# Optimization experiments

Measured on AMD Instinct MI355X. Metric: run time of the kernel, lower is better.

The kernel has to match this reference:

```python
import jax, jax.numpy as jnp
import numpy as np

VOCAB = 50000
EDIM = 128
CDIM = 128
B = 512
LEVEL_FACTORS = [4, 4, 3, 3, 2, 1]  # 7 levels total, N = 403968 nodes


def _build_forest():
    """Deterministic random forest: per-level arrays of token, global parent idx, depth, batch id."""
    rng = np.random.default_rng(0)
    level_sizes = [B]
    for f in LEVEL_FACTORS:
        level_sizes.append(level_sizes[-1] * f)
    offsets = np.cumsum([0] + level_sizes)
    tokens = [rng.integers(0, VOCAB, B)]
    parent = [np.zeros(B, np.int64)]          # roots: dummy parent (depth 0 never scattered)
    depth = [np.zeros(B, np.int64)]
    batch_id = [np.arange(B)]
    for d in range(1, len(level_sizes)):
        n = level_sizes[d]
        tokens.append(rng.integers(0, VOCAB, n))
        p_local = rng.integers(0, level_sizes[d - 1], n)
        parent.append(offsets[d - 1] + p_local)
        depth.append(np.full(n, d, np.int64))
        batch_id.append(batch_id[d - 1][p_local])
    cat = lambda xs: np.concatenate(xs).astype(np.int32)
    return cat(tokens), cat(parent), cat(depth), cat(batch_id), len(level_sizes)


def setup_inputs() -> dict:
    key = jax.random.key(0)
    k1, k2, k3 = jax.random.split(key, 3)
    emb_table = jax.random.normal(k1, (VOCAB, EDIM), dtype=jnp.float32) * 0.02
    W = jax.random.normal(k2, (CDIM, EDIM), dtype=jnp.float32) * 0.02
    b = jax.random.normal(k3, (CDIM,), dtype=jnp.float32) * 0.02
    tokens, parent, depth, batch_id, num_levels = _build_forest()
    return {
        "emb_table": emb_table,
        "W": W,
        "b": b,
        "tokens": jnp.asarray(tokens),
        "parent": jnp.asarray(parent),
        "depth": jnp.asarray(depth),
        "batch_id": jnp.asarray(batch_id),
        "num_levels": num_levels,
        "batch_size": B,
    }


def reference(emb_table, W, b, tokens, parent, depth, batch_id, num_levels, batch_size):
    N = tokens.shape[0]
    # per-node base: W_c(embedding(token))  [N, CDIM]
    base = emb_table[tokens] @ W.T + b
    h = base
    # bottom-up subtree sum, level-batched scatter-add (deepest level first)
    for d in range(num_levels - 1, 0, -1):
        contrib = jnp.where((depth == d)[:, None], h, 0.0)
        h = h + jax.ops.segment_sum(contrib, parent, num_segments=N)
    # per-batch elementwise max over all nodes of the tree, clamped at 0
    # (original maxes zero-initialized snapshots over all recursion calls)
    out = jax.ops.segment_max(h, batch_id, num_segments=batch_size)
    return jnp.maximum(out, 0.0)
```

## Files before the change

kernel.cpp:

```cpp
#include <hip/hip_runtime.h>
#include <hip/hip_bf16.h>


using f32x4   = __attribute__((ext_vector_type(4))) float;
using short8  = __attribute__((ext_vector_type(8))) short;
using ushort8 = __attribute__((ext_vector_type(8))) unsigned short;
using float4v = __attribute__((ext_vector_type(4))) float;

#define N_ALL   403968
#define N_NONRT 403456
#define N_PAR   256512
#define OFF1    512
#define OFF2    2560
#define OFF3    10752
#define OFF4    35328
#define OFF5    109056
#define OFF6    256512
#define NVOCAB  50000
#define CAP1    32
#define CAP2    32
#define CAP3    24
#define CAP4    24
#define CAP5    20
#define CAPL    16
#define D1CAP   24
#define D2CAP   64
#define WEMB_BLOCKS 782

__device__ __forceinline__ short f2bf(float f) {
  union { float f; unsigned u; } v; v.f = f;
  unsigned r = v.u + 0x7fffu + ((v.u >> 16) & 1u);
  return (short)(r >> 16);
}
__device__ __forceinline__ float bf2f(unsigned short u) {
  union { unsigned u; float f; } v; v.u = ((unsigned)u) << 16; return v.f;
}

__global__ __launch_bounds__(256) void prep_k(const float* __restrict__ W,
                                              const float* __restrict__ emb,
                                              const float* __restrict__ bias,
                                              unsigned short* __restrict__ Wemb,
                                              const int* __restrict__ parent,
                                              const int* __restrict__ tokens,
                                              int* __restrict__ cnt,
                                              int* __restrict__ L1,
                                              int* __restrict__ L2,
                                              int* __restrict__ L3,
                                              int* __restrict__ L4,
                                              unsigned long long* __restrict__ L5,
                                              unsigned short* __restrict__ LeafTok) {
  if (blockIdx.x >= WEMB_BLOCKS) {
    const int i = (blockIdx.x - WEMB_BLOCKS) * 256 + threadIdx.x + 512;
    const int p = parent[i];
    const int slot = atomicAdd(cnt + p, 1);
    if (i >= OFF6) {
      if (slot < CAPL)
        LeafTok[(size_t)(p - OFF5) * CAPL + slot] = (unsigned short)tokens[i];
    } else if (i >= OFF5) {
      if (slot < CAP5) {
        const unsigned long long v =
            ((unsigned long long)(unsigned)tokens[i] << 32) |
            (unsigned)(i - OFF5);
        L5[(size_t)(p - OFF4) * CAP5 + slot] = v;
      }
    } else if (i >= OFF4) {
      if (slot < CAP4) L4[(size_t)(p - OFF3) * CAP4 + slot] = i - OFF4;
    } else if (i >= OFF3) {
      if (slot < CAP3) L3[(size_t)(p - OFF2) * CAP3 + slot] = i - OFF3;
    } else if (i >= OFF2) {
      if (slot < CAP2) L2[(size_t)(p - OFF1) * CAP2 + slot] = i - OFF2;
    } else {
      if (slot < CAP1) L1[(size_t)p * CAP1 + slot] = i - OFF1;
    }
    return;
  }
  __shared__ short WBs[16384];
  for (int idx = threadIdx.x; idx < 16384; idx += 256) {
    int j = idx & 7, c16 = (idx >> 3) & 15, g = (idx >> 7) & 3,
        s = (idx >> 9) & 3, t = idx >> 11;
    WBs[idx] = f2bf(W[(t * 16 + c16) * 128 + s * 32 + g * 8 + j]);
  }
  __syncthreads();

  const int tid = threadIdx.x, lane = tid & 63, wv = tid >> 6;
  const int l15 = lane & 15, g = lane >> 4;
  const int nb = blockIdx.x * 64 + wv * 16;

  f32x4 acc[8];
  #pragma unroll
  for (int t = 0; t < 8; ++t) {
    const float bb = bias[t * 16 + l15];
    #pragma unroll
    for (int j = 0; j < 4; ++j) acc[t][j] = bb;
  }
  int vr = nb + l15; if (vr > NVOCAB - 1) vr = NVOCAB - 1;
  const float* erow = emb + (size_t)vr * 128;
  short8 a[4];
  #pragma unroll
  for (int s = 0; s < 4; ++s) {
    float4v f0 = *(const float4v*)(erow + s * 32 + g * 8);
    float4v f1 = *(const float4v*)(erow + s * 32 + g * 8 + 4);
    short8 t;
    t[0] = f2bf(f0[0]); t[1] = f2bf(f0[1]); t[2] = f2bf(f0[2]); t[3] = f2bf(f0[3]);
    t[4] = f2bf(f1[0]); t[5] = f2bf(f1[1]); t[6] = f2bf(f1[2]); t[7] = f2bf(f1[3]);
    a[s] = t;
  }
  #pragma unroll
  for (int t = 0; t < 8; ++t) {
    #pragma unroll
    for (int s = 0; s < 4; ++s) {
      const short8 bfr = *(const short8*)&WBs[((((t * 4 + s) * 4) + g) * 16 + l15) * 8];
      acc[t] = __builtin_amdgcn_mfma_f32_16x16x32_bf16(a[s], bfr, acc[t], 0, 0, 0);
    }
  }
  #pragma unroll
  for (int j = 0; j < 4; ++j) {
    const int r = nb + g * 4 + j;
    if (r < NVOCAB) {
      ushort8 hv;
      #pragma unroll
      for (int t = 0; t < 8; ++t) hv[t] = (unsigned short)f2bf(acc[t][j]);
      *(ushort8*)(Wemb + (size_t)r * 128 + l15 * 8) = hv;
    }
  }
}

__global__ __launch_bounds__(256, 8) void d4f_k(
    const unsigned short* __restrict__ Wemb,
    const int*   __restrict__ tokens,
    const int*   __restrict__ cnt,
    const unsigned long long* __restrict__ L5,
    const unsigned short* __restrict__ LeafTok,
    unsigned short* __restrict__ Hout)
{
  const int chunk = threadIdx.x & 15;
  const int node  = threadIdx.x >> 4;
  const int nd    = blockIdx.x * 16 + node;
  const int gid   = OFF4 + nd;

  float acc[8], mx[8];
  {
    const int tok = tokens[gid];
    const ushort8 b = *(const ushort8*)(Wemb + (size_t)tok * 128 + chunk * 8);
    #pragma unroll
    for (int t = 0; t < 8; ++t) { acc[t] = bf2f(b[t]); mx[t] = 0.0f; }
  }

  const int n5 = min(cnt[gid], CAP5);
  const size_t b5 = (size_t)nd * CAP5;
  for (int c = 0; c < n5; ++c) {
    const unsigned long long e5 = L5[b5 + c];
    const int tok5 = (int)(e5 >> 32);
    const int lid5 = (int)(e5 & 0xffffffffu);
    const int lc = min(cnt[OFF5 + lid5], CAPL);
    const size_t lb = (size_t)lid5 * CAPL;
    const ushort8 r5 = *(const ushort8*)(Wemb + (size_t)tok5 * 128 + chunk * 8);
    float h5[8], lmx[8];
    #pragma unroll
    for (int t = 0; t < 8; ++t) { h5[t] = bf2f(r5[t]); lmx[t] = 0.0f; }
    for (int l = 0; l < lc; ++l) {
      const int tl = LeafTok[lb + l];
      const ushort8 rl = *(const ushort8*)(Wemb + (size_t)tl * 128 + chunk * 8);
      #pragma unroll
      for (int t = 0; t < 8; ++t) {
        const float hv = bf2f(rl[t]);
        h5[t] += hv;
        lmx[t] = fmaxf(lmx[t], hv);
      }
    }
    #pragma unroll
    for (int t = 0; t < 8; ++t) {
      acc[t] += h5[t];
      mx[t] = fmaxf(mx[t], fmaxf(lmx[t], h5[t]));
    }
  }

  ushort8 hv, mv;
  #pragma unroll
  for (int t = 0; t < 8; ++t) {
    hv[t] = (unsigned short)f2bf(acc[t]);
    mv[t] = (unsigned short)f2bf(fmaxf(mx[t], acc[t]));
  }
  __builtin_nontemporal_store(hv, (ushort8*)(Hout + (size_t)nd * 256 + chunk * 8));
  __builtin_nontemporal_store(mv, (ushort8*)(Hout + (size_t)nd * 256 + 128 + chunk * 8));
}

__global__ __launch_bounds__(256, 8) void d3_k(
    const unsigned short* __restrict__ Wemb,
    const int*   __restrict__ tokens,
    const unsigned short* __restrict__ Hin,
    unsigned short*       __restrict__ Hout,
    const int*   __restrict__ cnt,
    const int*   __restrict__ L4)
{
  const int chunk = threadIdx.x & 15;
  const int node  = threadIdx.x >> 4;
  const int nd    = blockIdx.x * 16 + node;
  const int gid   = OFF3 + nd;

  float acc[8], mx[8];
  {
    const int tok = tokens[gid];
    const ushort8 b = *(const ushort8*)(Wemb + (size_t)tok * 128 + chunk * 8);
    #pragma unroll
    for (int t = 0; t < 8; ++t) { acc[t] = bf2f(b[t]); mx[t] = 0.0f; }
  }

  const int n4 = min(cnt[gid], CAP4);
  const size_t b4 = (size_t)nd * CAP4;
  int k = 0;
  for (; k + 2 <= n4; k += 2) {
    const int c0 = L4[b4 + k], c1 = L4[b4 + k + 1];
    const ushort8 h0 = *(const ushort8*)(Hin + (size_t)c0 * 256 + chunk * 8);
    const ushort8 m0 = *(const ushort8*)(Hin + (size_t)c0 * 256 + 128 + chunk * 8);
    const ushort8 h1 = *(const ushort8*)(Hin + (size_t)c1 * 256 + chunk * 8);
    const ushort8 m1 = *(const ushort8*)(Hin + (size_t)c1 * 256 + 128 + chunk * 8);
    #pragma unroll
    for (int t = 0; t < 8; ++t) {
      acc[t] += bf2f(h0[t]); mx[t] = fmaxf(mx[t], bf2f(m0[t]));
      acc[t] += bf2f(h1[t]); mx[t] = fmaxf(mx[t], bf2f(m1[t]));
    }
  }
  if (k < n4) {
    const int c0 = L4[b4 + k];
    const ushort8 h0 = *(const ushort8*)(Hin + (size_t)c0 * 256 + chunk * 8);
    const ushort8 m0 = *(const ushort8*)(Hin + (size_t)c0 * 256 + 128 + chunk * 8);
    #pragma unroll
    for (int t = 0; t < 8; ++t) {
      acc[t] += bf2f(h0[t]); mx[t] = fmaxf(mx[t], bf2f(m0[t]));
    }
  }

  ushort8 hv, mv;
  #pragma unroll
  for (int t = 0; t < 8; ++t) {
    hv[t] = (unsigned short)f2bf(acc[t]);
    mv[t] = (unsigned short)f2bf(fmaxf(mx[t], acc[t]));
  }
  *(ushort8*)(Hout + (size_t)nd * 256 + chunk * 8) = hv;
  *(ushort8*)(Hout + (size_t)nd * 256 + 128 + chunk * 8) = mv;
}

__global__ __launch_bounds__(256, 2) void top_k(
    const unsigned short* __restrict__ Wemb,
    const int*   __restrict__ tokens,
    const unsigned short* __restrict__ Hd3,
    float*       __restrict__ outf,
    const int*   __restrict__ cnt,
    const int*   __restrict__ L1,
    const int*   __restrict__ L2,
    const int*   __restrict__ L3)
{
  __shared__ int d1id[D1CAP];
  __shared__ int c2[D1CAP];
  __shared__ int d2off[D1CAP + 1];
  __shared__ int d2id[D2CAP];
  __shared__ int n2s;
  __shared__ unsigned short rec2[D2CAP][256];
  __shared__ unsigned short rec1[D1CAP][256];

  const int r   = blockIdx.x;
  const int tid = threadIdx.x;
  const int chunk = tid & 15, grp = tid >> 4;

  int n1 = min(cnt[r], D1CAP);
  if (tid < n1) {
    const int lid1 = L1[(size_t)r * CAP1 + tid];
    d1id[tid] = lid1;
    c2[tid] = min(cnt[OFF1 + lid1], CAP2);
  }
  __syncthreads();
  if (tid == 0) {
    int run = 0;
    for (int i = 0; i < n1; ++i) {
      d2off[i] = run; run += c2[i];
      if (run > D2CAP) run = D2CAP;
    }
    d2off[n1] = run; n2s = run;
  }
  __syncthreads();
  const int n2 = n2s;
  if (tid < n1) {
    const int lid1 = d1id[tid];
    const int o = d2off[tid], cmax = d2off[tid + 1] - o;
    for (int q = 0; q < cmax; ++q)
      d2id[o + q] = L2[(size_t)lid1 * CAP2 + q];
  }
  __syncthreads();

  for (int i = grp; i < n2; i += 16) {
    const int lid2 = d2id[i];
    float acc[8], mx[8];
    {
      const ushort8 b = *(const ushort8*)(Wemb + (size_t)tokens[OFF2 + lid2] * 128 + chunk * 8);
      #pragma unroll
      for (int t = 0; t < 8; ++t) { acc[t] = bf2f(b[t]); mx[t] = 0.0f; }
    }
    const int n3 = min(cnt[OFF2 + lid2], CAP3);
    for (int k = 0; k < n3; ++k) {
      const int lid3 = L3[(size_t)lid2 * CAP3 + k];
      const ushort8 h0 = *(const ushort8*)(Hd3 + (size_t)lid3 * 256 + chunk * 8);
      const ushort8 m0 = *(const ushort8*)(Hd3 + (size_t)lid3 * 256 + 128 + chunk * 8);
      #pragma unroll
      for (int t = 0; t < 8; ++t) {
        acc[t] += bf2f(h0[t]); mx[t] = fmaxf(mx[t], bf2f(m0[t]));
      }
    }
    #pragma unroll
    for (int t = 0; t < 8; ++t) {
      rec2[i][chunk * 8 + t] = (unsigned short)f2bf(acc[t]);
      rec2[i][128 + chunk * 8 + t] =
          (unsigned short)f2bf(fmaxf(mx[t], acc[t]));
    }
  }
  __syncthreads();

  for (int i = grp; i < n1; i += 16) {
    const int lid1 = d1id[i];
    float acc[8], mx[8];
    {
      const ushort8 b = *(const ushort8*)(Wemb + (size_t)tokens[OFF1 + lid1] * 128 + chunk * 8);
      #pragma unroll
      for (int t = 0; t < 8; ++t) { acc[t] = bf2f(b[t]); mx[t] = 0.0f; }
    }
    for (int q = d2off[i]; q < d2off[i + 1]; ++q) {
      #pragma unroll
      for (int t = 0; t < 8; ++t) {
        acc[t] += bf2f(rec2[q][chunk * 8 + t]);
        mx[t] = fmaxf(mx[t], bf2f(rec2[q][128 + chunk * 8 + t]));
      }
    }
    #pragma unroll
    for (int t = 0; t < 8; ++t) {
      rec1[i][chunk * 8 + t] = (unsigned short)f2bf(acc[t]);
      rec1[i][128 + chunk * 8 + t] =
          (unsigned short)f2bf(fmaxf(mx[t], acc[t]));
    }
  }
  __syncthreads();

  if (grp == 0) {
    float acc[8], mx[8];
    {
      const ushort8 b = *(const ushort8*)(Wemb + (size_t)tokens[r] * 128 + chunk * 8);
      #pragma unroll
      for (int t = 0; t < 8; ++t) { acc[t] = bf2f(b[t]); mx[t] = 0.0f; }
    }
    for (int i = 0; i < n1; ++i) {
      #pragma unroll
      for (int t = 0; t < 8; ++t) {
        acc[t] += bf2f(rec1[i][chunk * 8 + t]);
        mx[t] = fmaxf(mx[t], bf2f(rec1[i][128 + chunk * 8 + t]));
      }
    }
    #pragma unroll
    for (int t = 0; t < 8; ++t)
      outf[(size_t)r * 128 + t * 16 + chunk] = fmaxf(mx[t], acc[t]);
  }
}

extern "C" void kernel_launch(void* const* d_in, const int* in_sizes, int n_in,
                              void* d_out, int out_size, void* d_ws, size_t ws_size,
                              hipStream_t stream) {
  (void)in_sizes; (void)n_in; (void)out_size; (void)ws_size;

  const float* emb    = (const float*)d_in[0];
  const float* W      = (const float*)d_in[1];
  const float* bias   = (const float*)d_in[2];
  const int*   tokens = (const int*)d_in[3];
  const int*   parent = (const int*)d_in[4];

  char* p = (char*)d_ws;
  unsigned short* bufB = (unsigned short*)p;
  unsigned short* bufA = (unsigned short*)(p + 75497472);
  int* cnt     = (int*)(p + 115886084);
  unsigned short* Wemb = (unsigned short*)(p + 116949008);
  unsigned long long* L5 = (unsigned long long*)(p + 129749008);
  int* L4      = (int*)(p + 141545488);
  int* L3      = (int*)(p + 143904784);
  int* L2      = (int*)(p + 144691216);
  int* L1      = (int*)(p + 144953360);
  unsigned short* LeafTok = (unsigned short*)(p + 145018896);

  float* outf = (float*)d_out;

  hipMemsetAsync(cnt, 0, (size_t)N_PAR * 4, stream);
  prep_k<<<WEMB_BLOCKS + N_NONRT / 256, 256, 0, stream>>>(
      W, emb, bias, Wemb, parent, tokens, cnt,
      L1, L2, L3, L4, L5, LeafTok);

  d4f_k<<<73728 / 16, 256, 0, stream>>>(Wemb, tokens, cnt, L5, LeafTok, bufA);
  d3_k<<<24576 / 16, 256, 0, stream>>>(Wemb, tokens, bufA, bufB, cnt, L4);
  top_k<<<512, 256, 0, stream>>>(Wemb, tokens, bufB, outf, cnt, L1, L2, L3);
}
```

Before: 110.8 us.

## Split d4f feature dimension across four blocks with 32-bit gathers

The depth-4/5/6 fused kernel now handles each node's 128 features in four quarter-slices. Each lane loads one 32-bit word holding two bf16 values instead of a 16-byte vector, and the grid is four times larger. The block index is swizzled so that adjacent blocks share node groups, which should let the repeated index and token reads hit cache. This raises thread-level parallelism and latency hiding for the dependent gather chains, at the cost of redundant index/count loads per slice and narrower memory transactions.

```diff
diff --git a/kernel.cpp b/kernel.cpp
--- a/kernel.cpp
+++ b/kernel.cpp
@@ -34,6 +34,12 @@
 }
 __device__ __forceinline__ float bf2f(unsigned short u) {
   union { unsigned u; float f; } v; v.u = ((unsigned)u) << 16; return v.f;
+}
+__device__ __forceinline__ float lo_bf(unsigned v) {
+  union { unsigned u; float f; } x; x.u = v << 16; return x.f;
+}
+__device__ __forceinline__ float hi_bf(unsigned v) {
+  union { unsigned u; float f; } x; x.u = v & 0xffff0000u; return x.f;
 }
 
 __global__ __launch_bounds__(256) void prep_k(const float* __restrict__ W,
@@ -133,17 +139,22 @@
     const unsigned short* __restrict__ LeafTok,
     unsigned short* __restrict__ Hout)
 {
-  const int chunk = threadIdx.x & 15;
-  const int node  = threadIdx.x >> 4;
-  const int nd    = blockIdx.x * 16 + node;
-  const int gid   = OFF4 + nd;
-
-  float acc[8], mx[8];
+  const int b = blockIdx.x;
+  const int x = b & 7;
+  const int q = x >> 1;
+  const int nb16 = ((b >> 3) << 1) | (x & 1);
+  const int lane16 = threadIdx.x & 15;
+  const int node   = threadIdx.x >> 4;
+  const int nd  = nb16 * 16 + node;
+  const int gid = OFF4 + nd;
+
+  const unsigned* __restrict__ WembU = (const unsigned*)Wemb;
+  const int rofs = q * 16 + lane16;
+
+  float acc0, acc1, mx0 = 0.0f, mx1 = 0.0f;
   {
-    const int tok = tokens[gid];
-    const ushort8 b = *(const ushort8*)(Wemb + (size_t)tok * 128 + chunk * 8);
-    #pragma unroll
-    for (int t = 0; t < 8; ++t) { acc[t] = bf2f(b[t]); mx[t] = 0.0f; }
+    const unsigned bv = WembU[(size_t)tokens[gid] * 64 + rofs];
+    acc0 = lo_bf(bv); acc1 = hi_bf(bv);
   }
 
   const int n5 = min(cnt[gid], CAP5);
@@ -154,35 +165,28 @@
     const int lid5 = (int)(e5 & 0xffffffffu);
     const int lc = min(cnt[OFF5 + lid5], CAPL);
     const size_t lb = (size_t)lid5 * CAPL;
-    const ushort8 r5 = *(const ushort8*)(Wemb + (size_t)tok5 * 128 + chunk * 8);
-    float h5[8], lmx[8];
-    #pragma unroll
-    for (int t = 0; t < 8; ++t) { h5[t] = bf2f(r5[t]); lmx[t] = 0.0f; }
+    const unsigned r5 = WembU[(size_t)tok5 * 64 + rofs];
+    float h0 = lo_bf(r5), h1 = hi_bf(r5);
+    float l0 = 0.0f, l1 = 0.0f;
     for (int l = 0; l < lc; ++l) {
       const int tl = LeafTok[lb + l];
-      const ushort8 rl = *(const ushort8*)(Wemb + (size_t)tl * 128 + chunk * 8);
-      #pragma unroll
-      for (int t = 0; t < 8; ++t) {
-        const float hv = bf2f(rl[t]);
-        h5[t] += hv;
-        lmx[t] = fmaxf(lmx[t], hv);
-      }
-    }
-    #pragma unroll
-    for (int t = 0; t < 8; ++t) {
-      acc[t] += h5[t];
-      mx[t] = fmaxf(mx[t], fmaxf(lmx[t], h5[t]));
-    }
-  }
-
-  ushort8 hv, mv;
-  #pragma unroll
-  for (int t = 0; t < 8; ++t) {
-    hv[t] = (unsigned short)f2bf(acc[t]);
-    mv[t] = (unsigned short)f2bf(fmaxf(mx[t], acc[t]));
-  }
-  __builtin_nontemporal_store(hv, (ushort8*)(Hout + (size_t)nd * 256 + chunk * 8));
-  __builtin_nontemporal_store(mv, (ushort8*)(Hout + (size_t)nd * 256 + 128 + chunk * 8));
+      const unsigned rl = WembU[(size_t)tl * 64 + rofs];
+      const float f0 = lo_bf(rl), f1 = hi_bf(rl);
+      h0 += f0; h1 += f1;
+      l0 = fmaxf(l0, f0); l1 = fmaxf(l1, f1);
+    }
+    acc0 += h0; acc1 += h1;
+    mx0 = fmaxf(mx0, fmaxf(l0, h0));
+    mx1 = fmaxf(mx1, fmaxf(l1, h1));
+  }
+
+  const unsigned ph = ((unsigned)(unsigned short)f2bf(acc1) << 16) |
+                      (unsigned)(unsigned short)f2bf(acc0);
+  const unsigned pm = ((unsigned)(unsigned short)f2bf(fmaxf(mx1, acc1)) << 16) |
+                      (unsigned)(unsigned short)f2bf(fmaxf(mx0, acc0));
+  unsigned* HoutU = (unsigned*)Hout;
+  __builtin_nontemporal_store(ph, HoutU + (size_t)nd * 128 + rofs);
+  __builtin_nontemporal_store(pm, HoutU + (size_t)nd * 128 + 64 + rofs);
 }
 
 __global__ __launch_bounds__(256, 8) void d3_k(
@@ -389,7 +393,7 @@
       W, emb, bias, Wemb, parent, tokens, cnt,
       L1, L2, L3, L4, L5, LeafTok);
 
-  d4f_k<<<73728 / 16, 256, 0, stream>>>(Wemb, tokens, cnt, L5, LeafTok, bufA);
+  d4f_k<<<(73728 / 16) * 4, 256, 0, stream>>>(Wemb, tokens, cnt, L5, LeafTok, bufA);
   d3_k<<<24576 / 16, 256, 0, stream>>>(Wemb, tokens, bufA, bufB, cnt, L4);
   top_k<<<512, 256, 0, stream>>>(Wemb, tokens, bufB, outf, cnt, L1, L2, L3);
 }
```

Result: slower. 157.8 us (+42.4%).
